# Kernel optimization log

Hardware: AMD Instinct MI355X
Metric: run time of the kernel (lower is better)

Reference implementation:

```python
import jax, jax.numpy as jnp
import numpy as np

VOCAB = 50000
EMB = 512
HID = 512
OUT = 2
B = 64
T = 512

def setup_inputs() -> dict:
    key = jax.random.key(0)
    k1, k2, k3, k4, k5, k6 = jax.random.split(key, 6)
    x = jax.random.randint(k1, (B, T), 0, VOCAB, dtype=jnp.int32)
    emb = jax.random.normal(k2, (VOCAB, EMB), dtype=jnp.float32) * 0.02
    emb = emb.at[0].set(0.0)  # padding_idx row zeroed
    W1 = jax.random.normal(k3, (HID, 2 * EMB), dtype=jnp.float32) * (1.0 / np.sqrt(2 * EMB))
    b1 = jax.random.normal(k4, (HID,), dtype=jnp.float32) * 0.01
    W2 = jax.random.normal(k5, (OUT, HID), dtype=jnp.float32) * (1.0 / np.sqrt(HID))
    b2 = jax.random.normal(k6, (OUT,), dtype=jnp.float32) * 0.01
    return {"x": x, "emb": emb, "W1": W1, "b1": b1, "W2": W2, "b2": b2}

def reference(x, emb, W1, b1, W2, b2):
    xe = emb[x]                      # [B, T, E]
    h0 = jnp.zeros((x.shape[0], emb.shape[1]), dtype=emb.dtype)

    def step(h, xt):                 # xt: [B, E], h: [B, H]
        inp = jnp.concatenate([xt, h], axis=1)        # [B, 2E]
        h_new = jnp.tanh(inp @ W1.T + b1)             # [B, H]
        return h_new, h_new

    hT, outs = jax.lax.scan(step, h0, jnp.swapaxes(xe, 0, 1))  # outs: [T, B, H]
    pooled = jnp.max(outs, axis=0)                    # max over time -> [B, H]
    logits = pooled @ W2.T + b2                       # [B, OUT]
    return logits, hT
```

## Files before the change

kernel.cpp:

```cpp
#include <hip/hip_runtime.h>
#include <math.h>

#define TT   512
#define BB   64
#define EMBD 512
#define HIDD 512

typedef _Float16 half2v __attribute__((ext_vector_type(2)));
typedef _Float16 half8  __attribute__((ext_vector_type(8)));
typedef float    f32x4  __attribute__((ext_vector_type(4)));

__device__ __forceinline__ float fdot2(unsigned a, unsigned b, float c) {
  half2v av = __builtin_bit_cast(half2v, a);
  half2v bv = __builtin_bit_cast(half2v, b);
  return __builtin_amdgcn_fdot2(av, bv, c, false);
}

__device__ __forceinline__ float fast_tanh(float x) {
  float e = __expf(2.0f * x);
  return 1.0f - 2.0f * __builtin_amdgcn_rcpf(e + 1.0f);
}

__device__ __forceinline__ unsigned pack2(float a, float b) {
  half2v hv; hv.x = (_Float16)a; hv.y = (_Float16)b;
  return __builtin_bit_cast(unsigned, hv);
}

__device__ __forceinline__ uint4 pack8(float4 f0, float4 f1) {
  uint4 u;
  u.x = pack2(f0.x, f0.y); u.y = pack2(f0.z, f0.w);
  u.z = pack2(f1.x, f1.y); u.w = pack2(f1.z, f1.w);
  return u;
}

__global__ __launch_bounds__(256) void repack_w1h(
    const float* __restrict__ W1, uint4* __restrict__ wp)
{
  const int gid = blockIdx.x * 256 + threadIdx.x;
  const int c   = gid >> 9;
  const int tid = gid & 511;
  const int w = tid >> 6, l = tid & 63;
  const int qa = l >> 4, jg = l & 15;
  const int jo = c & 3, kq = c >> 2;
  const int j  = 64 * w + 4 * jg + jo;
  const int k0 = 128 * qa + 8 * kq;
  const float* src = W1 + (size_t)j * (2 * EMBD) + EMBD + k0;
  unsigned r[4];
#pragma unroll
  for (int q = 0; q < 4; q++) r[q] = pack2(src[2 * q], src[2 * q + 1]);
  uint4 u; u.x = r[0]; u.y = r[1]; u.z = r[2]; u.w = r[3];
  wp[gid] = u;
}

__global__ __launch_bounds__(256, 1) void px_mfma(
    const int* __restrict__ xx, const float* __restrict__ emb,
    const float* __restrict__ W1, const float* __restrict__ b1,
    float* __restrict__ px)
{
  __shared__ uint4 At[128 * 16];
  __shared__ uint4 Bt[256 * 16];
  __shared__ int stok[128];

  const int tid = threadIdx.x;
  const int wv  = tid >> 6, l = tid & 63;
  const int m0  = blockIdx.x * 128;
  const int j0  = blockIdx.y * 256;

  if (tid < 128) stok[tid] = xx[m0 + tid];

  f32x4 acc[8][4];
#pragma unroll
  for (int q = 0; q < 4; q++) {
    const float bc = b1[j0 + wv * 64 + 16 * q + (l & 15)];
#pragma unroll
    for (int i = 0; i < 8; i++) { acc[i][q].x = bc; acc[i][q].y = bc; acc[i][q].z = bc; acc[i][q].w = bc; }
  }

  for (int kc = 0; kc < 4; kc++) {
    __syncthreads();
    {
      const int r = tid >> 1, h = tid & 1;
      const float4* s4 = (const float4*)(emb + (size_t)stok[r] * EMBD + kc * 128 + h * 64);
#pragma unroll
      for (int i = 0; i < 8; i++)
        At[r * 16 + ((8 * h + i) ^ (r & 15))] = pack8(s4[2 * i], s4[2 * i + 1]);
      const float4* t4 = (const float4*)(W1 + (size_t)(j0 + tid) * (2 * EMBD) + kc * 128);
#pragma unroll
      for (int i = 0; i < 16; i++)
        Bt[tid * 16 + (i ^ (tid & 15))] = pack8(t4[2 * i], t4[2 * i + 1]);
    }
    __syncthreads();

#pragma unroll
    for (int ks = 0; ks < 4; ks++) {
      const int so = ks * 4 + (l >> 4);
      half8 a[8], bfr[4];
#pragma unroll
      for (int i = 0; i < 8; i++) {
        const int ra = 16 * i + (l & 15);
        a[i] = __builtin_bit_cast(half8, At[ra * 16 + (so ^ (ra & 15))]);
      }
#pragma unroll
      for (int q = 0; q < 4; q++) {
        const int rb = wv * 64 + 16 * q + (l & 15);
        bfr[q] = __builtin_bit_cast(half8, Bt[rb * 16 + (so ^ (rb & 15))]);
      }
#pragma unroll
      for (int i = 0; i < 8; i++)
#pragma unroll
        for (int q = 0; q < 4; q++)
          acc[i][q] = __builtin_amdgcn_mfma_f32_16x16x32_f16(a[i], bfr[q], acc[i][q], 0, 0, 0);
    }
  }

#pragma unroll
  for (int i = 0; i < 8; i++) {
    const int mrow = m0 + 16 * i + (l >> 4) * 4;
#pragma unroll
    for (int q = 0; q < 4; q++) {
      const int col = j0 + wv * 64 + 16 * q + (l & 15);
      float* dst = px + (size_t)mrow * HIDD + col;
      dst[0 * HIDD] = acc[i][q].x;
      dst[1 * HIDD] = acc[i][q].y;
      dst[2 * HIDD] = acc[i][q].z;
      dst[3 * HIDD] = acc[i][q].w;
    }
  }
}

#define DOT4(HH, W0, W1v, W2v, W3v) do {                                    \
    const uint4 hh = (HH);                                                  \
    a0=fdot2((W0).x,hh.x,a0);  a0=fdot2((W0).y,hh.y,a0);                    \
    a0=fdot2((W0).z,hh.z,a0);  a0=fdot2((W0).w,hh.w,a0);                    \
    a1=fdot2((W1v).x,hh.x,a1); a1=fdot2((W1v).y,hh.y,a1);                   \
    a1=fdot2((W1v).z,hh.z,a1); a1=fdot2((W1v).w,hh.w,a1);                   \
    a2=fdot2((W2v).x,hh.x,a2); a2=fdot2((W2v).y,hh.y,a2);                   \
    a2=fdot2((W2v).z,hh.z,a2); a2=fdot2((W2v).w,hh.w,a2);                   \
    a3=fdot2((W3v).x,hh.x,a3); a3=fdot2((W3v).y,hh.y,a3);                   \
    a3=fdot2((W3v).z,hh.z,a3); a3=fdot2((W3v).w,hh.w,a3);                   \
  } while (0)

__attribute__((amdgpu_flat_work_group_size(512, 512), amdgpu_waves_per_eu(2)))
__global__ void elman_v10(
    const uint4* __restrict__ wp, const float* __restrict__ px,
    const float* __restrict__ W2, const float* __restrict__ b2,
    float* __restrict__ out)
{
  __shared__ uint4 wlds[15 * 512];
  __shared__ uint4 h2[2][64];
  __shared__ float red[2][8];

  const int b   = blockIdx.x;
  const int tid = threadIdx.x;
  const int w   = tid >> 6, l = tid & 63;
  const int qa  = l >> 4, jg = l & 15;

  uint4 wr[49];
#pragma unroll
  for (int i = 0; i < 49; i++) wr[i] = wp[(size_t)i * 512 + tid];
#pragma unroll
  for (int i = 0; i < 15; i++) wlds[i * 512 + tid] = wp[(size_t)(49 + i) * 512 + tid];
  if (tid < 64) {
    uint4 z; z.x = z.y = z.z = z.w = 0u;
    h2[0][tid] = z;
  }
  __syncthreads();

  const float* pxb = px + (size_t)b * TT * HIDD;
  float rm0 = -INFINITY, rm1 = -INFINITY, rm2 = -INFINITY, rm3 = -INFINITY;

  for (int t = 0; t < TT; t++) {
    const int cur = t & 1;

    float4 pxv = make_float4(0.f, 0.f, 0.f, 0.f);
    if (l < 16)
      pxv = *(const float4*)(pxb + (size_t)t * HIDD + 64 * w + 4 * jg);

    const uint4* hb = &h2[cur][0];
    float a0 = 0.f, a1 = 0.f, a2 = 0.f, a3 = 0.f;

#pragma unroll
    for (int kq = 0; kq < 12; kq++)
      DOT4(hb[kq * 4 + qa], wr[4 * kq + 0], wr[4 * kq + 1], wr[4 * kq + 2], wr[4 * kq + 3]);
    DOT4(hb[12 * 4 + qa], wr[48],
         wlds[0 * 512 + tid], wlds[1 * 512 + tid], wlds[2 * 512 + tid]);
    DOT4(hb[13 * 4 + qa], wlds[3 * 512 + tid], wlds[4 * 512 + tid],
         wlds[5 * 512 + tid], wlds[6 * 512 + tid]);
    DOT4(hb[14 * 4 + qa], wlds[7 * 512 + tid], wlds[8 * 512 + tid],
         wlds[9 * 512 + tid], wlds[10 * 512 + tid]);
    DOT4(hb[15 * 4 + qa], wlds[11 * 512 + tid], wlds[12 * 512 + tid],
         wlds[13 * 512 + tid], wlds[14 * 512 + tid]);

    a0 += __shfl_xor(a0, 16); a1 += __shfl_xor(a1, 16);
    a2 += __shfl_xor(a2, 16); a3 += __shfl_xor(a3, 16);
    a0 += __shfl_xor(a0, 32); a1 += __shfl_xor(a1, 32);
    a2 += __shfl_xor(a2, 32); a3 += __shfl_xor(a3, 32);

    if (l < 16) {
      float h0 = fast_tanh(a0 + pxv.x);
      float h1 = fast_tanh(a1 + pxv.y);
      float h2n = fast_tanh(a2 + pxv.z);
      float h3 = fast_tanh(a3 + pxv.w);
      rm0 = fmaxf(rm0, h0); rm1 = fmaxf(rm1, h1);
      rm2 = fmaxf(rm2, h2n); rm3 = fmaxf(rm3, h3);
      const int qw  = w >> 1;
      const int kqw = (w & 1) * 8 + (jg >> 1);
      const int di  = (kqw * 4 + qw) * 4 + (jg & 1) * 2;
      unsigned* hw = (unsigned*)&h2[cur ^ 1][0];
      *(uint2*)&hw[di] = make_uint2(pack2(h0, h1), pack2(h2n, h3));
      if (t == TT - 1)
        *(float4*)(out + 2 * BB + (size_t)b * HIDD + 64 * w + 4 * jg) =
            make_float4(h0, h1, h2n, h3);
    }
    __syncthreads();
  }

  float* pl = (float*)wlds;
  if (l < 16)
    *(float4*)&pl[64 * w + 4 * jg] = make_float4(rm0, rm1, rm2, rm3);
  __syncthreads();
  {
    float pv = pl[tid];
    float q0 = pv * W2[tid];
    float q1 = pv * W2[HIDD + tid];
#pragma unroll
    for (int off = 32; off; off >>= 1) {
      q0 += __shfl_down(q0, off);
      q1 += __shfl_down(q1, off);
    }
    if (l == 0) { red[0][w] = q0; red[1][w] = q1; }
  }
  __syncthreads();
  if (tid < 2) {
    float s = b2[tid];
#pragma unroll
    for (int i = 0; i < 8; i++) s += red[tid][i];
    out[b * 2 + tid] = s;
  }
}

extern "C" void kernel_launch(void* const* d_in, const int* in_sizes, int n_in,
                              void* d_out, int out_size, void* d_ws, size_t ws_size,
                              hipStream_t stream)
{
  const int*   x   = (const int*)d_in[0];
  const float* emb = (const float*)d_in[1];
  const float* W1  = (const float*)d_in[2];
  const float* b1  = (const float*)d_in[3];
  const float* W2  = (const float*)d_in[4];
  const float* b2  = (const float*)d_in[5];
  float* out = (float*)d_out;
  char* ws = (char*)d_ws;

  uint4* wp = (uint4*)ws;
  float* px = (float*)(ws + (1 << 19));
  const size_t need = (size_t)(1 << 19) + (size_t)BB * TT * HIDD * sizeof(float);
  if (ws_size < need) return;

  repack_w1h<<<128, 256, 0, stream>>>(W1, wp);
  px_mfma<<<dim3(TT * BB / 128, HIDD / 256), 256, 0, stream>>>(x, emb, W1, b1, px);
  elman_v10<<<dim3(BB), dim3(512), 0, stream>>>(wp, px, W2, b2, out);
}
```

Baseline: 855.3 us.

## Replace shuffle reduction with LDS partial-sum reduction and per-thread tanh in recurrence

Changes the work split of the recurrent matvec. Each wave now covers a contiguous k-quarter for 256 outputs, and the weights are repacked to match. The 4 k-quarter partial sums are written to LDS and summed by every thread, so all 512 threads compute one tanh each instead of 16 lanes per wave computing four, and the cross-lane shuffle reduction goes away. The cost is a second barrier per timestep and extra LDS traffic for the partial sums.

```diff
diff --git a/kernel.cpp b/kernel.cpp
--- a/kernel.cpp
+++ b/kernel.cpp
@@ -40,14 +40,14 @@
   const int c   = gid >> 9;
   const int tid = gid & 511;
   const int w = tid >> 6, l = tid & 63;
-  const int qa = l >> 4, jg = l & 15;
+  const int q = w & 3, hh = w >> 2;
   const int jo = c & 3, kq = c >> 2;
-  const int j  = 64 * w + 4 * jg + jo;
-  const int k0 = 128 * qa + 8 * kq;
+  const int j  = 256 * hh + 4 * l + jo;
+  const int k0 = 128 * q + 8 * kq;
   const float* src = W1 + (size_t)j * (2 * EMBD) + EMBD + k0;
   unsigned r[4];
 #pragma unroll
-  for (int q = 0; q < 4; q++) r[q] = pack2(src[2 * q], src[2 * q + 1]);
+  for (int p = 0; p < 4; p++) r[p] = pack2(src[2 * p], src[2 * p + 1]);
   uint4 u; u.x = r[0]; u.y = r[1]; u.z = r[2]; u.w = r[3];
   wp[gid] = u;
 }
@@ -141,88 +141,68 @@
   } while (0)
 
 __attribute__((amdgpu_flat_work_group_size(512, 512), amdgpu_waves_per_eu(2)))
-__global__ void elman_v10(
+__global__ void elman_v11(
     const uint4* __restrict__ wp, const float* __restrict__ px,
     const float* __restrict__ W2, const float* __restrict__ b2,
     float* __restrict__ out)
 {
   __shared__ uint4 wlds[15 * 512];
-  __shared__ uint4 h2[2][64];
+  __shared__ __align__(16) unsigned short hbuf[HIDD];
+  __shared__ float parts[4][HIDD];
   __shared__ float red[2][8];
 
   const int b   = blockIdx.x;
   const int tid = threadIdx.x;
   const int w   = tid >> 6, l = tid & 63;
-  const int qa  = l >> 4, jg = l & 15;
+  const int q   = w & 3;
+  const int hh  = w >> 2;
+  const int jb  = 256 * hh + 4 * l;
 
   uint4 wr[49];
 #pragma unroll
   for (int i = 0; i < 49; i++) wr[i] = wp[(size_t)i * 512 + tid];
 #pragma unroll
   for (int i = 0; i < 15; i++) wlds[i * 512 + tid] = wp[(size_t)(49 + i) * 512 + tid];
-  if (tid < 64) {
-    uint4 z; z.x = z.y = z.z = z.w = 0u;
-    h2[0][tid] = z;
-  }
+  if (tid < 64) ((uint4*)hbuf)[tid] = make_uint4(0u, 0u, 0u, 0u);
   __syncthreads();
 
-  const float* pxb = px + (size_t)b * TT * HIDD;
-  float rm0 = -INFINITY, rm1 = -INFINITY, rm2 = -INFINITY, rm3 = -INFINITY;
+  const uint4* hq = (const uint4*)hbuf + 16 * q;
+  const float* pxj = px + (size_t)b * TT * HIDD + tid;
+  float rmq = -INFINITY;
 
   for (int t = 0; t < TT; t++) {
-    const int cur = t & 1;
-
-    float4 pxv = make_float4(0.f, 0.f, 0.f, 0.f);
-    if (l < 16)
-      pxv = *(const float4*)(pxb + (size_t)t * HIDD + 64 * w + 4 * jg);
-
-    const uint4* hb = &h2[cur][0];
+    float pxs = pxj[(size_t)t * HIDD];
+
     float a0 = 0.f, a1 = 0.f, a2 = 0.f, a3 = 0.f;
 
 #pragma unroll
     for (int kq = 0; kq < 12; kq++)
-      DOT4(hb[kq * 4 + qa], wr[4 * kq + 0], wr[4 * kq + 1], wr[4 * kq + 2], wr[4 * kq + 3]);
-    DOT4(hb[12 * 4 + qa], wr[48],
+      DOT4(hq[kq], wr[4 * kq + 0], wr[4 * kq + 1], wr[4 * kq + 2], wr[4 * kq + 3]);
+    DOT4(hq[12], wr[48],
          wlds[0 * 512 + tid], wlds[1 * 512 + tid], wlds[2 * 512 + tid]);
-    DOT4(hb[13 * 4 + qa], wlds[3 * 512 + tid], wlds[4 * 512 + tid],
+    DOT4(hq[13], wlds[3 * 512 + tid], wlds[4 * 512 + tid],
          wlds[5 * 512 + tid], wlds[6 * 512 + tid]);
-    DOT4(hb[14 * 4 + qa], wlds[7 * 512 + tid], wlds[8 * 512 + tid],
+    DOT4(hq[14], wlds[7 * 512 + tid], wlds[8 * 512 + tid],
          wlds[9 * 512 + tid], wlds[10 * 512 + tid]);
-    DOT4(hb[15 * 4 + qa], wlds[11 * 512 + tid], wlds[12 * 512 + tid],
+    DOT4(hq[15], wlds[11 * 512 + tid], wlds[12 * 512 + tid],
          wlds[13 * 512 + tid], wlds[14 * 512 + tid]);
 
-    a0 += __shfl_xor(a0, 16); a1 += __shfl_xor(a1, 16);
-    a2 += __shfl_xor(a2, 16); a3 += __shfl_xor(a3, 16);
-    a0 += __shfl_xor(a0, 32); a1 += __shfl_xor(a1, 32);
-    a2 += __shfl_xor(a2, 32); a3 += __shfl_xor(a3, 32);
-
-    if (l < 16) {
-      float h0 = fast_tanh(a0 + pxv.x);
-      float h1 = fast_tanh(a1 + pxv.y);
-      float h2n = fast_tanh(a2 + pxv.z);
-      float h3 = fast_tanh(a3 + pxv.w);
-      rm0 = fmaxf(rm0, h0); rm1 = fmaxf(rm1, h1);
-      rm2 = fmaxf(rm2, h2n); rm3 = fmaxf(rm3, h3);
-      const int qw  = w >> 1;
-      const int kqw = (w & 1) * 8 + (jg >> 1);
-      const int di  = (kqw * 4 + qw) * 4 + (jg & 1) * 2;
-      unsigned* hw = (unsigned*)&h2[cur ^ 1][0];
-      *(uint2*)&hw[di] = make_uint2(pack2(h0, h1), pack2(h2n, h3));
-      if (t == TT - 1)
-        *(float4*)(out + 2 * BB + (size_t)b * HIDD + 64 * w + 4 * jg) =
-            make_float4(h0, h1, h2n, h3);
-    }
-    __syncthreads();
-  }
-
-  float* pl = (float*)wlds;
-  if (l < 16)
-    *(float4*)&pl[64 * w + 4 * jg] = make_float4(rm0, rm1, rm2, rm3);
-  __syncthreads();
+    *(float4*)&parts[q][jb] = make_float4(a0, a1, a2, a3);
+    __syncthreads();
+
+    float s = parts[0][tid] + parts[1][tid] + parts[2][tid] + parts[3][tid] + pxs;
+    float hv = fast_tanh(s);
+    rmq = fmaxf(rmq, hv);
+    _Float16 hf = (_Float16)hv;
+    hbuf[tid] = __builtin_bit_cast(unsigned short, hf);
+    if (t == TT - 1)
+      out[2 * BB + (size_t)b * HIDD + tid] = hv;
+    __syncthreads();
+  }
+
   {
-    float pv = pl[tid];
-    float q0 = pv * W2[tid];
-    float q1 = pv * W2[HIDD + tid];
+    float q0 = rmq * W2[tid];
+    float q1 = rmq * W2[HIDD + tid];
 #pragma unroll
     for (int off = 32; off; off >>= 1) {
       q0 += __shfl_down(q0, off);
@@ -259,5 +239,5 @@
 
   repack_w1h<<<128, 256, 0, stream>>>(W1, wp);
   px_mfma<<<dim3(TT * BB / 128, HIDD / 256), 256, 0, stream>>>(x, emb, W1, b1, px);
-  elman_v10<<<dim3(BB), dim3(512), 0, stream>>>(wp, px, W2, b2, out);
-}
+  elman_v11<<<dim3(BB), dim3(512), 0, stream>>>(wp, px, W2, b2, out);
+}
```

After: 805.9 us. -5.8%, faster.
